# Kernel tuning notes

Measured on AMD Instinct MI355X. Metric: run time of the kernel, lower is better.

Reference implementation:

```python
import jax, jax.numpy as jnp
import numpy as np

E, D, H = 8, 2048, 2048  # num_experts, features, expert_dim
B, L, K = 2, 2048, 2


def setup_inputs() -> dict:
    key = jax.random.key(0)
    k1, k2, k3, k4, k5, k6 = jax.random.split(key, 6)
    x = jax.random.normal(k1, (B, L, D), dtype=jnp.float32)
    w = jax.random.uniform(k2, (B, L, K), dtype=jnp.float32)
    weights = w / jnp.sum(w, axis=-1, keepdims=True)  # normalised routing weights
    expert_indices = jax.random.randint(k3, (B, L, K), 0, E, dtype=jnp.int64)
    gate_up = jax.random.normal(k4, (E, D, 2 * H), dtype=jnp.float32) * 0.02
    down = jax.random.normal(k5, (E, H, D), dtype=jnp.float32) * 0.02
    per_expert_scale = 1.0 + 0.01 * jax.random.normal(k6, (E,), dtype=jnp.float32)
    return {"x": x, "weights": weights, "expert_indices": expert_indices,
            "gate_up": gate_up, "down": down, "per_expert_scale": per_expert_scale}


def reference(x, weights, expert_indices, gate_up, down, per_expert_scale):
    Bb, Ll, Dd = x.shape
    Ee = gate_up.shape[0]
    N = Bb * Ll
    xf = x.reshape(N, Dd)                                   # [N, D]
    idx = expert_indices.reshape(N, -1)                     # [N, K]
    wts = weights.reshape(N, -1)                            # [N, K]
    # combine[n, e] = sum_k weights[n,k] * 1[idx[n,k]==e]; scale folded in.
    onehot = jax.nn.one_hot(idx, Ee, dtype=x.dtype)         # [N, K, E]
    combine = jnp.einsum('nk,nke->ne', wts, onehot) * per_expert_scale  # [N, E]
    # Dense per-expert GatedMLP (grouped GEMM across all experts).
    h = jnp.einsum('nd,edh->enh', xf, gate_up)              # [E, N, 2H]
    gate, up = jnp.split(h, 2, axis=-1)
    act = jax.nn.gelu(gate, approximate=False) * up         # exact gelu, as torch F.gelu
    y = jnp.einsum('enh,ehd->end', act, down)               # [E, N, D]
    out = jnp.einsum('end,ne->nd', y, combine)              # weighted combine over experts
    return out.reshape(Bb, Ll, Dd)
```

## Files before the change

### kernel.cpp

```cpp
#include <hip/hip_runtime.h>
#include <math.h>

#define EXPERTS 8
#define DDIM 2048
#define HDIM 2048
#define NTOK 4096
#define NPAIR 8192
#define MAXSLOT 9216
#define MAXTILE 72

typedef _Float16 f16;
typedef __attribute__((ext_vector_type(8))) _Float16 f16x8;
typedef __attribute__((ext_vector_type(4))) _Float16 f16x4;
typedef __attribute__((ext_vector_type(4))) float f32x4;

#define GUPT_OFF 0ull
#define Y_OFF    0ull
#define DWNT_OFF 41943040ull
#define XF_OFF   134217728ull
#define ACT_OFF  150994944ull
#define CTRL_OFF 192937984ull
#define CTRL_INTS 26792

#define BARRIER() asm volatile("s_barrier" ::: "memory")
#define VMCNT(n)  asm volatile("s_waitcnt vmcnt(" #n ")" ::: "memory")

__device__ __forceinline__ void gload_lds16(const void* g, void* l) {
  __builtin_amdgcn_global_load_lds(
      (const __attribute__((address_space(1))) unsigned int*)g,
      (__attribute__((address_space(3))) unsigned int*)l,
      16, 0, 0);
}

__global__ void k_detect(const int* __restrict__ w, int* flag) {
  int i = blockIdx.x * blockDim.x + threadIdx.x;
  if (i < NPAIR / 2 && w[2 * i + 1] != 0) atomicOr(flag, 1);
}

__device__ __forceinline__ int expert_of(const int* idx, int is32, int p) {
  return is32 ? idx[p] : idx[2 * p];
}

__global__ void k_count(const int* __restrict__ idx, const int* __restrict__ flag,
                        int* cnt) {
  int p = blockIdx.x * blockDim.x + threadIdx.x;
  if (p < NPAIR) atomicAdd(&cnt[expert_of(idx, *flag, p)], 1);
}

__global__ void k_plan(const int* __restrict__ cnt, int* cursor,
                       int* tile_e, int* tile_r0, int* n_tiles) {
  if (blockIdx.x == 0 && threadIdx.x == 0) {
    int off = 0, nt = 0;
    for (int e = 0; e < EXPERTS; ++e) {
      cursor[e] = off;
      int t = (cnt[e] + 127) >> 7;
      for (int i = 0; i < t; ++i) { tile_e[nt] = e; tile_r0[nt] = off + i * 128; ++nt; }
      off += t * 128;
    }
    *n_tiles = nt;
  }
}

__global__ void k_assign(const int* __restrict__ idx, const int* __restrict__ flag,
                         const float* __restrict__ wts, const float* __restrict__ scale,
                         int* cursor, int* slot_tok, int* tok_slot, float* slot_w) {
  int p = blockIdx.x * blockDim.x + threadIdx.x;
  if (p < NPAIR) {
    int e = expert_of(idx, *flag, p);
    int pos = atomicAdd(&cursor[e], 1);
    slot_tok[pos] = p >> 1;
    tok_slot[p] = pos;
    slot_w[pos] = wts[p] * scale[e];
  }
}

__global__ void k_cvt_x(const float* __restrict__ in, f16* __restrict__ out) {
  int i = blockIdx.x * blockDim.x + threadIdx.x;
  float4 v = ((const float4*)in)[i];
  f16x4 o = {(f16)v.x, (f16)v.y, (f16)v.z, (f16)v.w};
  ((f16x4*)out)[i] = o;
}

__global__ __launch_bounds__(256) void k_transpose(const float* __restrict__ in,
                                                   f16* __restrict__ out,
                                                   int R, int C) {
  __shared__ float t[64][65];
  const size_t base = (size_t)blockIdx.z * R * C;
  const float* ip = in + base;
  f16* op = out + base;
  const int c0 = blockIdx.x * 64, r0 = blockIdx.y * 64;
  const int tid = threadIdx.x;
  const int rr = tid >> 4, cc = (tid & 15) * 4;
#pragma unroll
  for (int i = 0; i < 4; ++i) {
    float4 v = *(const float4*)&ip[(size_t)(r0 + rr + i * 16) * C + c0 + cc];
    *(float4*)&t[rr + i * 16][cc] = v;
  }
  __syncthreads();
  const int k0 = (tid & 7) * 8;
#pragma unroll
  for (int p = 0; p < 2; ++p) {
    const int j = (tid >> 3) + p * 32;
    f16x8 w = {(f16)t[k0 + 0][j], (f16)t[k0 + 1][j], (f16)t[k0 + 2][j],
               (f16)t[k0 + 3][j], (f16)t[k0 + 4][j], (f16)t[k0 + 5][j],
               (f16)t[k0 + 6][j], (f16)t[k0 + 7][j]};
    *(f16x8*)&op[(size_t)(c0 + j) * R + r0 + k0] = w;
  }
}

template <int G1>
__global__ __launch_bounds__(256, 2) void k_gemm(
    const f16* __restrict__ Asrc, const f16* __restrict__ Bsrc,
    const int* __restrict__ slot_tok,
    const int* __restrict__ tile_e, const int* __restrict__ tile_r0,
    const int* __restrict__ n_tiles, f16* __restrict__ dst) {
  __shared__ __align__(16) f16 smem[2][16384];

  const int NTX = G1 ? 32 : 16;
  const int GP = NTX / 8;
  const int oid = (int)(blockIdx.y * NTX + blockIdx.x);
  const int nt = (oid & 7) * GP + ((oid >> 3) & (GP - 1));
  const int bx = oid >> (G1 ? 5 : 4);
  if (bx >= *n_tiles) return;
  const int e = tile_e[bx];
  const int m0 = tile_r0[bx];

  const int tid = threadIdx.x;
  const int lane = tid & 63;
  const int wv = tid >> 6;
  const int wrM = wv >> 1;
  const int wn = wv & 1;
  const int fr = lane & 15;
  const int fhi = lane >> 4;

  const int sr = tid >> 3;
  const f16* aS[4];
  const f16* bS[4];
#pragma unroll
  for (int i = 0; i < 4; ++i) {
    const int r = i * 32 + sr;
    const int sc = (tid & 7) ^ (r & 7);
    size_t arow = G1 ? (size_t)slot_tok[m0 + r] : (size_t)(m0 + r);
    aS[i] = Asrc + arow * 2048 + sc * 8;
    size_t brow;
    if (G1) brow = (size_t)e * 4096 + (r < 64 ? (size_t)(nt * 64 + r)
                                              : (size_t)(2048 + nt * 64 + r - 64));
    else    brow = (size_t)e * 2048 + nt * 128 + r;
    bS[i] = Bsrc + brow * 2048 + sc * 8;
  }
  auto stageA = [&](int s, int kt) {
#pragma unroll
    for (int i = 0; i < 4; ++i)
      gload_lds16(aS[i] + (size_t)kt * 64, &smem[s][i * 2048 + tid * 8]);
  };
  auto stageB = [&](int s, int kt) {
#pragma unroll
    for (int i = 0; i < 4; ++i)
      gload_lds16(bS[i] + (size_t)kt * 64, &smem[s][8192 + i * 2048 + tid * 8]);
  };

  int ctv[4];
#pragma unroll
  for (int ci = 0; ci < 4; ++ci) {
    if (G1) ctv[ci] = (ci < 2) ? (wn * 2 + ci) : (4 + wn * 2 + (ci - 2));
    else    ctv[ci] = wn * 4 + ci;
  }

  f32x4 acc[4][4];
#pragma unroll
  for (int i = 0; i < 4; ++i)
#pragma unroll
    for (int j = 0; j < 4; ++j) acc[i][j] = (f32x4){0.f, 0.f, 0.f, 0.f};

  const int NT = 32;

  stageB(0, 0);
  stageA(0, 0);
  stageB(1, 1);
  VMCNT(4);
  BARRIER();

  for (int kt = 0; kt < NT; ++kt) {
    const int s = kt & 1;
    if (kt + 1 < NT) stageA(s ^ 1, kt + 1);

    const f16* As = &smem[s][0];
    const f16* Bs = &smem[s][8192];
    f16x8 bf[4][2];
#pragma unroll
    for (int ci = 0; ci < 4; ++ci)
#pragma unroll
      for (int k0 = 0; k0 < 2; ++k0) {
        const int c = ctv[ci] * 16 + fr;
        bf[ci][k0] = *(const f16x8*)&Bs[c * 64 + (((k0 * 4 + fhi) ^ (c & 7)) << 3)];
      }
#pragma unroll
    for (int mi = 0; mi < 2; ++mi) {
      f16x8 af[2];
#pragma unroll
      for (int k0 = 0; k0 < 2; ++k0) {
        const int r = wrM * 64 + mi * 16 + fr;
        af[k0] = *(const f16x8*)&As[r * 64 + (((k0 * 4 + fhi) ^ (r & 7)) << 3)];
      }
      __builtin_amdgcn_s_setprio(1);
#pragma unroll
      for (int ci = 0; ci < 4; ++ci)
#pragma unroll
        for (int k0 = 0; k0 < 2; ++k0)
          acc[mi][ci] = __builtin_amdgcn_mfma_f32_16x16x32_f16(
              af[k0], bf[ci][k0], acc[mi][ci], 0, 0, 0);
      __builtin_amdgcn_s_setprio(0);
    }
    BARRIER();
    if (kt + 2 < NT) stageB(s, kt + 2);
#pragma unroll
    for (int mi = 2; mi < 4; ++mi) {
      f16x8 af[2];
#pragma unroll
      for (int k0 = 0; k0 < 2; ++k0) {
        const int r = wrM * 64 + mi * 16 + fr;
        af[k0] = *(const f16x8*)&As[r * 64 + (((k0 * 4 + fhi) ^ (r & 7)) << 3)];
      }
      __builtin_amdgcn_s_setprio(1);
#pragma unroll
      for (int ci = 0; ci < 4; ++ci)
#pragma unroll
        for (int k0 = 0; k0 < 2; ++k0)
          acc[mi][ci] = __builtin_amdgcn_mfma_f32_16x16x32_f16(
              af[k0], bf[ci][k0], acc[mi][ci], 0, 0, 0);
      __builtin_amdgcn_s_setprio(0);
    }
    if (kt + 1 < NT) {
      if (kt + 2 < NT) { VMCNT(4); } else { VMCNT(0); }
      BARRIER();
    }
  }

  if (G1) {
#pragma unroll
    for (int mi = 0; mi < 4; ++mi)
#pragma unroll
      for (int ci = 0; ci < 2; ++ci)
#pragma unroll
        for (int rg = 0; rg < 4; ++rg) {
          const int row = m0 + wrM * 64 + mi * 16 + fhi * 4 + rg;
          const int col = nt * 64 + (wn * 2 + ci) * 16 + fr;
          const float g = acc[mi][ci][rg];
          const float u = acc[mi][ci + 2][rg];
          const float a = 0.5f * g * (1.0f + erff(g * 0.70710678118654752f)) * u;
          dst[(size_t)row * 2048 + col] = (f16)a;
        }
  } else {
#pragma unroll
    for (int mi = 0; mi < 4; ++mi)
#pragma unroll
      for (int ci = 0; ci < 4; ++ci)
#pragma unroll
        for (int rg = 0; rg < 4; ++rg) {
          const int row = m0 + wrM * 64 + mi * 16 + fhi * 4 + rg;
          const int col = nt * 128 + (wn * 4 + ci) * 16 + fr;
          dst[(size_t)row * 2048 + col] = (f16)acc[mi][ci][rg];
        }
  }
}

__global__ void k_combine(const f16* __restrict__ y, const float* __restrict__ slot_w,
                          const int* __restrict__ tok_slot, float* __restrict__ out) {
  const int gid = blockIdx.x * blockDim.x + threadIdx.x;
  const int tok = gid >> 8;
  const int c = (gid & 255) * 8;
  const int s0 = tok_slot[2 * tok], s1 = tok_slot[2 * tok + 1];
  const float w0 = slot_w[s0], w1 = slot_w[s1];
  const f16x8 v0 = *(const f16x8*)&y[(size_t)s0 * 2048 + c];
  const f16x8 v1 = *(const f16x8*)&y[(size_t)s1 * 2048 + c];
  float o[8];
#pragma unroll
  for (int j = 0; j < 8; ++j) o[j] = w0 * (float)v0[j] + w1 * (float)v1[j];
  float4* op = (float4*)&out[(size_t)tok * 2048 + c];
  op[0] = (float4){o[0], o[1], o[2], o[3]};
  op[1] = (float4){o[4], o[5], o[6], o[7]};
}

extern "C" void kernel_launch(void* const* d_in, const int* in_sizes, int n_in,
                              void* d_out, int out_size, void* d_ws, size_t ws_size,
                              hipStream_t stream) {
  const float* x = (const float*)d_in[0];
  const float* wts = (const float*)d_in[1];
  const int* idx = (const int*)d_in[2];
  const float* gup = (const float*)d_in[3];
  const float* dwn = (const float*)d_in[4];
  const float* scale = (const float*)d_in[5];
  float* out = (float*)d_out;

  char* ws = (char*)d_ws;
  f16* gup_t = (f16*)(ws + GUPT_OFF);
  f16* y = (f16*)(ws + Y_OFF);
  f16* down_t = (f16*)(ws + DWNT_OFF);
  f16* xf = (f16*)(ws + XF_OFF);
  f16* act = (f16*)(ws + ACT_OFF);
  int* ctrl = (int*)(ws + CTRL_OFF);
  int* slot_tok = ctrl;
  int* tok_slot = ctrl + 9216;
  int* cnt = ctrl + 17408;
  int* cursor = ctrl + 17416;
  int* tile_e = ctrl + 17424;
  int* tile_r0 = ctrl + 17496;
  int* n_tiles = ctrl + 17568;
  int* is32 = ctrl + 17569;
  float* slot_w = (float*)(ctrl + 17576);

  hipMemsetAsync(ctrl, 0, (size_t)CTRL_INTS * sizeof(int), stream);

  k_detect<<<NPAIR / 2 / 256, 256, 0, stream>>>(idx, is32);
  k_count<<<NPAIR / 256, 256, 0, stream>>>(idx, is32, cnt);
  k_plan<<<1, 1, 0, stream>>>(cnt, cursor, tile_e, tile_r0, n_tiles);
  k_assign<<<NPAIR / 256, 256, 0, stream>>>(idx, is32, wts, scale, cursor,
                                            slot_tok, tok_slot, slot_w);
  k_cvt_x<<<NTOK * DDIM / 4 / 256, 256, 0, stream>>>(x, xf);
  k_transpose<<<dim3(4096 / 64, 2048 / 64, EXPERTS), 256, 0, stream>>>(
      gup, gup_t, 2048, 4096);
  k_gemm<1><<<dim3(32, MAXTILE), 256, 0, stream>>>(xf, gup_t, slot_tok, tile_e,
                                                   tile_r0, n_tiles, act);
  k_transpose<<<dim3(2048 / 64, 2048 / 64, EXPERTS), 256, 0, stream>>>(
      dwn, down_t, 2048, 2048);
  k_gemm<0><<<dim3(16, MAXTILE), 256, 0, stream>>>(act, down_t, slot_tok, tile_e,
                                                   tile_r0, n_tiles, y);
  k_combine<<<NTOK, 256, 0, stream>>>(y, slot_w, tok_slot, out);
}
```

Before: 465.1 us.

## Widen GEMM tiles to 128x256 with 8 waves and halve K-step to 32

The grouped GEMM block grows from 256 to 512 threads (8 waves), and the output tile widens from 128x128 to 128x256 columns, so each A tile is reused across more B columns and fewer blocks are launched. The K-step per pipeline stage drops from 64 to 32 to keep shared memory at 48KB per block, with the LDS swizzle reworked for 32-wide rows. The cost is twice as many loop iterations and barriers, with fewer MFMAs between each barrier. Launch bounds now request 4 blocks of 512 threads, which may force register pressure on the 64 accumulator floats.

New measurement: 482.5 us. +3.7%, slower.

```diff
diff --git a/kernel.cpp b/kernel.cpp
--- a/kernel.cpp
+++ b/kernel.cpp
@@ -109,18 +109,18 @@
 }
 
 template <int G1>
-__global__ __launch_bounds__(256, 2) void k_gemm(
+__global__ __launch_bounds__(512, 4) void k_gemm(
     const f16* __restrict__ Asrc, const f16* __restrict__ Bsrc,
     const int* __restrict__ slot_tok,
     const int* __restrict__ tile_e, const int* __restrict__ tile_r0,
     const int* __restrict__ n_tiles, f16* __restrict__ dst) {
-  __shared__ __align__(16) f16 smem[2][16384];
-
-  const int NTX = G1 ? 32 : 16;
+  __shared__ __align__(16) f16 smem[2][12288];
+
+  const int NTX = G1 ? 16 : 8;
   const int GP = NTX / 8;
   const int oid = (int)(blockIdx.y * NTX + blockIdx.x);
   const int nt = (oid & 7) * GP + ((oid >> 3) & (GP - 1));
-  const int bx = oid >> (G1 ? 5 : 4);
+  const int bx = oid >> (G1 ? 4 : 3);
   if (bx >= *n_tiles) return;
   const int e = tile_e[bx];
   const int m0 = tile_r0[bx];
@@ -128,41 +128,40 @@
   const int tid = threadIdx.x;
   const int lane = tid & 63;
   const int wv = tid >> 6;
-  const int wrM = wv >> 1;
-  const int wn = wv & 1;
+  const int wrM = wv >> 2;
+  const int wn = wv & 3;
   const int fr = lane & 15;
   const int fhi = lane >> 4;
 
-  const int sr = tid >> 3;
-  const f16* aS[4];
-  const f16* bS[4];
-#pragma unroll
-  for (int i = 0; i < 4; ++i) {
-    const int r = i * 32 + sr;
-    const int sc = (tid & 7) ^ (r & 7);
-    size_t arow = G1 ? (size_t)slot_tok[m0 + r] : (size_t)(m0 + r);
-    aS[i] = Asrc + arow * 2048 + sc * 8;
+  const int ar = tid >> 2;
+  const int asc = (tid & 3) ^ ((ar >> 1) & 3);
+  size_t arow0 = G1 ? (size_t)slot_tok[m0 + ar] : (size_t)(m0 + ar);
+  const f16* aS = Asrc + arow0 * 2048 + asc * 8;
+  auto stageA = [&](int s, int kt) {
+    gload_lds16(aS + (size_t)kt * 32, &smem[s][tid * 8]);
+  };
+
+  const f16* bS[2];
+#pragma unroll
+  for (int i = 0; i < 2; ++i) {
+    const int rl = i * 128 + (tid >> 2);
+    const int sc = (tid & 3) ^ ((rl >> 1) & 3);
     size_t brow;
-    if (G1) brow = (size_t)e * 4096 + (r < 64 ? (size_t)(nt * 64 + r)
-                                              : (size_t)(2048 + nt * 64 + r - 64));
-    else    brow = (size_t)e * 2048 + nt * 128 + r;
+    if (G1) brow = (size_t)e * 4096 + (rl < 128 ? (size_t)(nt * 128 + rl)
+                                                : (size_t)(2048 + nt * 128 + rl - 128));
+    else    brow = (size_t)e * 2048 + nt * 256 + rl;
     bS[i] = Bsrc + brow * 2048 + sc * 8;
   }
-  auto stageA = [&](int s, int kt) {
-#pragma unroll
-    for (int i = 0; i < 4; ++i)
-      gload_lds16(aS[i] + (size_t)kt * 64, &smem[s][i * 2048 + tid * 8]);
+  auto stageB = [&](int s, int kt) {
+#pragma unroll
+    for (int i = 0; i < 2; ++i)
+      gload_lds16(bS[i] + (size_t)kt * 32, &smem[s][4096 + i * 4096 + tid * 8]);
   };
-  auto stageB = [&](int s, int kt) {
-#pragma unroll
-    for (int i = 0; i < 4; ++i)
-      gload_lds16(bS[i] + (size_t)kt * 64, &smem[s][8192 + i * 2048 + tid * 8]);
-  };
 
   int ctv[4];
 #pragma unroll
   for (int ci = 0; ci < 4; ++ci) {
-    if (G1) ctv[ci] = (ci < 2) ? (wn * 2 + ci) : (4 + wn * 2 + (ci - 2));
+    if (G1) ctv[ci] = (ci < 2) ? (wn * 2 + ci) : (8 + wn * 2 + (ci - 2));
     else    ctv[ci] = wn * 4 + ci;
   }
 
@@ -172,12 +171,12 @@
 #pragma unroll
     for (int j = 0; j < 4; ++j) acc[i][j] = (f32x4){0.f, 0.f, 0.f, 0.f};
 
-  const int NT = 32;
+  const int NT = 64;
 
   stageB(0, 0);
   stageA(0, 0);
   stageB(1, 1);
-  VMCNT(4);
+  VMCNT(2);
   BARRIER();
 
   for (int kt = 0; kt < NT; ++kt) {
@@ -185,53 +184,39 @@
     if (kt + 1 < NT) stageA(s ^ 1, kt + 1);
 
     const f16* As = &smem[s][0];
-    const f16* Bs = &smem[s][8192];
-    f16x8 bf[4][2];
-#pragma unroll
-    for (int ci = 0; ci < 4; ++ci)
-#pragma unroll
-      for (int k0 = 0; k0 < 2; ++k0) {
-        const int c = ctv[ci] * 16 + fr;
-        bf[ci][k0] = *(const f16x8*)&Bs[c * 64 + (((k0 * 4 + fhi) ^ (c & 7)) << 3)];
-      }
+    const f16* Bs = &smem[s][4096];
+    f16x8 bf[4];
+#pragma unroll
+    for (int ci = 0; ci < 4; ++ci) {
+      const int c = ctv[ci] * 16 + fr;
+      bf[ci] = *(const f16x8*)&Bs[c * 32 + ((fhi ^ ((c >> 1) & 3)) << 3)];
+    }
 #pragma unroll
     for (int mi = 0; mi < 2; ++mi) {
-      f16x8 af[2];
-#pragma unroll
-      for (int k0 = 0; k0 < 2; ++k0) {
-        const int r = wrM * 64 + mi * 16 + fr;
-        af[k0] = *(const f16x8*)&As[r * 64 + (((k0 * 4 + fhi) ^ (r & 7)) << 3)];
-      }
+      const int r = wrM * 64 + mi * 16 + fr;
+      const f16x8 af = *(const f16x8*)&As[r * 32 + ((fhi ^ ((r >> 1) & 3)) << 3)];
       __builtin_amdgcn_s_setprio(1);
 #pragma unroll
       for (int ci = 0; ci < 4; ++ci)
-#pragma unroll
-        for (int k0 = 0; k0 < 2; ++k0)
-          acc[mi][ci] = __builtin_amdgcn_mfma_f32_16x16x32_f16(
-              af[k0], bf[ci][k0], acc[mi][ci], 0, 0, 0);
+        acc[mi][ci] = __builtin_amdgcn_mfma_f32_16x16x32_f16(af, bf[ci],
+                                                             acc[mi][ci], 0, 0, 0);
       __builtin_amdgcn_s_setprio(0);
     }
     BARRIER();
     if (kt + 2 < NT) stageB(s, kt + 2);
 #pragma unroll
     for (int mi = 2; mi < 4; ++mi) {
-      f16x8 af[2];
-#pragma unroll
-      for (int k0 = 0; k0 < 2; ++k0) {
-        const int r = wrM * 64 + mi * 16 + fr;
-        af[k0] = *(const f16x8*)&As[r * 64 + (((k0 * 4 + fhi) ^ (r & 7)) << 3)];
-      }
+      const int r = wrM * 64 + mi * 16 + fr;
+      const f16x8 af = *(const f16x8*)&As[r * 32 + ((fhi ^ ((r >> 1) & 3)) << 3)];
       __builtin_amdgcn_s_setprio(1);
 #pragma unroll
       for (int ci = 0; ci < 4; ++ci)
-#pragma unroll
-        for (int k0 = 0; k0 < 2; ++k0)
-          acc[mi][ci] = __builtin_amdgcn_mfma_f32_16x16x32_f16(
-              af[k0], bf[ci][k0], acc[mi][ci], 0, 0, 0);
+        acc[mi][ci] = __builtin_amdgcn_mfma_f32_16x16x32_f16(af, bf[ci],
+                                                             acc[mi][ci], 0, 0, 0);
       __builtin_amdgcn_s_setprio(0);
     }
     if (kt + 1 < NT) {
-      if (kt + 2 < NT) { VMCNT(4); } else { VMCNT(0); }
+      if (kt + 2 < NT) { VMCNT(2); } else { VMCNT(0); }
       BARRIER();
     }
   }
@@ -244,7 +229,7 @@
 #pragma unroll
         for (int rg = 0; rg < 4; ++rg) {
           const int row = m0 + wrM * 64 + mi * 16 + fhi * 4 + rg;
-          const int col = nt * 64 + (wn * 2 + ci) * 16 + fr;
+          const int col = nt * 128 + (wn * 2 + ci) * 16 + fr;
           const float g = acc[mi][ci][rg];
           const float u = acc[mi][ci + 2][rg];
           const float a = 0.5f * g * (1.0f + erff(g * 0.70710678118654752f)) * u;
@@ -258,7 +243,7 @@
 #pragma unroll
         for (int rg = 0; rg < 4; ++rg) {
           const int row = m0 + wrM * 64 + mi * 16 + fhi * 4 + rg;
-          const int col = nt * 128 + (wn * 4 + ci) * 16 + fr;
+          const int col = nt * 256 + (wn * 4 + ci) * 16 + fr;
           dst[(size_t)row * 2048 + col] = (f16)acc[mi][ci][rg];
         }
   }
@@ -319,11 +304,11 @@
   k_cvt_x<<<NTOK * DDIM / 4 / 256, 256, 0, stream>>>(x, xf);
   k_transpose<<<dim3(4096 / 64, 2048 / 64, EXPERTS), 256, 0, stream>>>(
       gup, gup_t, 2048, 4096);
-  k_gemm<1><<<dim3(32, MAXTILE), 256, 0, stream>>>(xf, gup_t, slot_tok, tile_e,
+  k_gemm<1><<<dim3(16, MAXTILE), 512, 0, stream>>>(xf, gup_t, slot_tok, tile_e,
                                                    tile_r0, n_tiles, act);
   k_transpose<<<dim3(2048 / 64, 2048 / 64, EXPERTS), 256, 0, stream>>>(
       dwn, down_t, 2048, 2048);
-  k_gemm<0><<<dim3(16, MAXTILE), 256, 0, stream>>>(act, down_t, slot_tok, tile_e,
-                                                   tile_r0, n_tiles, y);
+  k_gemm<0><<<dim3(8, MAXTILE), 512, 0, stream>>>(act, down_t, slot_tok, tile_e,
+                                                  tile_r0, n_tiles, y);
   k_combine<<<NTOK, 256, 0, stream>>>(y, slot_w, tok_slot, out);
 }
```
